# Performance work log

Measured on AMD Instinct MI355X. Metric: run time of the kernel, lower is better.

## Reference

```python
import jax, jax.numpy as jnp
import numpy as np

K = 5          # lbp kernel_size (odd)
POOL = 2       # pool_size
C = 64         # input channels
B, H, W = 8, 256, 256
OUT_CH = 1
NEG_SLOPE = 0.01
LN_EPS = 1e-5


def _idx_pairs(k):
    pairs = [([0, i], [k - 1, k - 1 - i]) for i in range(k)]
    pairs += [([i, k - 1], [k - 1 - i, 0]) for i in range(1, k - 1)]
    return pairs  # 2K-2 pairs


def setup_inputs() -> dict:
    key = jax.random.key(0)
    k1, k2, k3 = jax.random.split(key, 3)
    x = jax.random.normal(k1, (B, C, H, W), dtype=jnp.float32)
    m = 2 * K - 2
    conv_w = jax.random.normal(k2, (OUT_CH, m), dtype=jnp.float32) / np.float32(np.sqrt(m))
    conv_b = jax.random.normal(k3, (OUT_CH,), dtype=jnp.float32) * 0.01
    return {"x": x, "conv_w": conv_w, "conv_b": conv_b}


def _avg_pool(x):
    # torch avg_pool2d(kernel=POOL, stride=1, padding=POOL//2, count_include_pad=True)
    p = POOL // 2
    s = jax.lax.reduce_window(x, jnp.float32(0.0), jax.lax.add,
                              (1, 1, POOL, POOL), (1, 1, 1, 1),
                              ((0, 0), (0, 0), (p, p), (p, p)))
    return s / jnp.float32(POOL * POOL)


def reference(x, conv_w, conv_b):
    xp = _avg_pool(x)                 # [B, C, H+1, W+1]
    # Each lbp kernel plane is (+1 center, -1 at offset) replicated over all C
    # input channels, so the conv reduces to shifts of the channel sum.
    xs = xp.sum(axis=1)               # [B, H', W']
    pad = K // 2
    Hp, Wp = xs.shape[-2], xs.shape[-1]
    xs_pad = jnp.pad(xs, ((0, 0), (pad, pad), (pad, pad)))

    def shift(rc):
        r, c = rc
        return xs_pad[:, r:r + Hp, c:c + Wp]

    # (conv even ch) - (conv odd ch) = shift(idx1) - shift(idx0)
    feats = jnp.stack([shift(b) - shift(a) for a, b in _idx_pairs(K)], axis=1)  # [B, 2K-2, H', W']
    y = jnp.einsum('bmhw,om->bohw', feats, conv_w) + conv_b[None, :, None, None]
    # layer_norm over last two dims, no affine
    mu = y.mean(axis=(-2, -1), keepdims=True)
    var = ((y - mu) ** 2).mean(axis=(-2, -1), keepdims=True)
    y = (y - mu) / jnp.sqrt(var + LN_EPS)
    return jnp.where(y >= 0, y, NEG_SLOPE * y)
```

## Files before the change

### kernel.cpp

```cpp
#include <hip/hip_runtime.h>
#include <math.h>

#define BB 8
#define CC 64
#define HH 256
#define WW 256
#define HP 257
#define NPB (HP * HP)
#define NBLK ((NPB + 255) / 256)

#define SROWS 262
#define SSTR  264
#define SPIMG (SROWS * SSTR)

#define OFF_PART 0
#define OFF_Y    4352
#define OFF_SPAD (OFF_Y + BB * NPB)

#define N_INT (BB * 16384)
#define PAD_PER_IMG 908
#define N_TOT (N_INT + BB * PAD_PER_IMG)

__global__ __launch_bounds__(256) void k_chansum(const float* __restrict__ x,
                                                 float* __restrict__ ws) {
    int tid = blockIdx.x * 256 + threadIdx.x;
    float4* sp4 = reinterpret_cast<float4*>(ws + OFF_SPAD);
    if (tid < N_INT) {
        int b = tid >> 14;
        int p = tid & 16383;
        int i = p >> 6;
        int j4 = p & 63;
        const float4* xp = reinterpret_cast<const float4*>(x)
                           + (size_t)b * (CC * 16384) + p;
        float4 acc = make_float4(0.f, 0.f, 0.f, 0.f);
#pragma unroll 16
        for (int c = 0; c < CC; ++c) {
            float4 v = xp[(size_t)c * 16384];
            acc.x += v.x; acc.y += v.y; acc.z += v.z; acc.w += v.w;
        }
        sp4[b * (SPIMG / 4) + (i + 3) * (SSTR / 4) + 1 + j4] = acc;
    } else {
        int j = tid - N_INT;
        if (j < BB * PAD_PER_IMG) {
            int img = j / PAD_PER_IMG;
            int k = j % PAD_PER_IMG;
            int row, col4;
            if (k < 396) {
                int r = k / 66;
                row = (r < 3) ? r : 256 + r;
                col4 = k % 66;
            } else {
                int k2 = k - 396;
                row = 3 + (k2 >> 1);
                col4 = (k2 & 1) ? 65 : 0;
            }
            sp4[img * (SPIMG / 4) + row * (SSTR / 4) + col4] =
                make_float4(0.f, 0.f, 0.f, 0.f);
        }
    }
}

__device__ __forceinline__ void build_w(const float* __restrict__ cw, float W[6][6]) {
    float T[5][5];
#pragma unroll
    for (int i = 0; i < 5; ++i)
#pragma unroll
        for (int j = 0; j < 5; ++j) T[i][j] = 0.f;
#pragma unroll
    for (int d = 0; d < 5; ++d) { T[0][d] = -cw[d]; T[4][d] = cw[4 - d]; }
    T[1][4] = -cw[5]; T[2][4] = -cw[6]; T[3][4] = -cw[7];
    T[1][0] =  cw[7]; T[2][0] =  cw[6]; T[3][0] =  cw[5];
#pragma unroll
    for (int u = 0; u < 6; ++u)
#pragma unroll
        for (int v = 0; v < 6; ++v) {
            float a = 0.f;
#pragma unroll
            for (int dr = u - 1; dr <= u; ++dr)
#pragma unroll
                for (int dc = v - 1; dc <= v; ++dc)
                    if (dr >= 0 && dr < 5 && dc >= 0 && dc < 5) a += T[dr][dc];
            W[u][v] = 0.25f * a;
        }
}

__global__ __launch_bounds__(256) void k_conv(float* __restrict__ ws,
                                              const float* __restrict__ cw,
                                              const float* __restrict__ cbp) {
    int b = blockIdx.y;
    int e = blockIdx.x * 256 + threadIdx.x;
    float W[6][6];
    build_w(cw, W);
    float y = 0.f;
    if (e < NPB) {
        int h = e / HP, w = e % HP;
        const float* p = ws + OFF_SPAD + b * SPIMG + h * SSTR + w + 1;
        float acc = cbp[0];
#pragma unroll
        for (int u = 0; u < 6; ++u)
#pragma unroll
            for (int v = 0; v < 6; ++v)
                acc += W[u][v] * p[u * SSTR + v];
        y = acc;
        ws[OFF_Y + b * NPB + e] = y;
    }
    float v1 = y, v2 = y * y;
    for (int off = 32; off > 0; off >>= 1) {
        v1 += __shfl_down(v1, off);
        v2 += __shfl_down(v2, off);
    }
    __shared__ float red[8];
    int lane = threadIdx.x & 63, wid = threadIdx.x >> 6;
    if (lane == 0) { red[wid] = v1; red[4 + wid] = v2; }
    __syncthreads();
    if (threadIdx.x == 0) {
        ws[OFF_PART + b * NBLK + blockIdx.x] = red[0] + red[1] + red[2] + red[3];
        ws[OFF_PART + BB * NBLK + b * NBLK + blockIdx.x] =
            red[4] + red[5] + red[6] + red[7];
    }
}

__global__ __launch_bounds__(256) void k_final(const float* __restrict__ ws,
                                               float* __restrict__ out) {
    int b = blockIdx.y;
    float v1 = 0.f, v2 = 0.f;
    for (int i = threadIdx.x; i < NBLK; i += 256) {
        v1 += ws[OFF_PART + b * NBLK + i];
        v2 += ws[OFF_PART + BB * NBLK + b * NBLK + i];
    }
    for (int off = 32; off > 0; off >>= 1) {
        v1 += __shfl_down(v1, off);
        v2 += __shfl_down(v2, off);
    }
    __shared__ float red[8];
    __shared__ float st[2];
    int lane = threadIdx.x & 63, wid = threadIdx.x >> 6;
    if (lane == 0) { red[wid] = v1; red[4 + wid] = v2; }
    __syncthreads();
    if (threadIdx.x == 0) {
        float s1 = red[0] + red[1] + red[2] + red[3];
        float s2 = red[4] + red[5] + red[6] + red[7];
        float mu = s1 / (float)NPB;
        float var = s2 / (float)NPB - mu * mu;
        st[0] = mu;
        st[1] = 1.0f / sqrtf(var + 1e-5f);
    }
    __syncthreads();
    float mu = st[0], rs = st[1];
    int e = blockIdx.x * 256 + threadIdx.x;
    if (e < NPB) {
        float z = (ws[OFF_Y + b * NPB + e] - mu) * rs;
        out[b * NPB + e] = (z >= 0.f) ? z : 0.01f * z;
    }
}

extern "C" void kernel_launch(void* const* d_in, const int* in_sizes, int n_in,
                              void* d_out, int out_size, void* d_ws, size_t ws_size,
                              hipStream_t stream) {
    const float* x  = (const float*)d_in[0];
    const float* cw = (const float*)d_in[1];
    const float* cb = (const float*)d_in[2];
    float* out = (float*)d_out;
    float* ws  = (float*)d_ws;

    k_chansum<<<(N_TOT + 255) / 256, 256, 0, stream>>>(x, ws);
    dim3 g(NBLK, BB);
    k_conv<<<g, 256, 0, stream>>>(ws, cw, cb);
    k_final<<<g, 256, 0, stream>>>(ws, out);
}
```

Measured before the change: 202.3 us.

## Fuse three kernels into one cooperative kernel with grid syncs

Merges the channel-sum, conv and normalize kernels into a single cooperative launch of 512 blocks, separated by grid-wide barriers. Conv results stay in registers across the second barrier, so the intermediate y buffer is never written to or read back from global memory, and two launch gaps disappear. In exchange the channel-sum phase runs on a fixed 512-block grid with a grid-stride loop instead of a grid sized to the work, which may lower memory-level parallelism in that bandwidth-bound phase. Each grid.sync also costs something.

```diff
diff --git a/kernel.cpp b/kernel.cpp
--- a/kernel.cpp
+++ b/kernel.cpp
@@ -1,5 +1,8 @@
 #include <hip/hip_runtime.h>
+#include <hip/hip_cooperative_groups.h>
 #include <math.h>
+
+namespace cg = cooperative_groups;
 
 #define BB 8
 #define CC 64
@@ -7,58 +10,22 @@
 #define WW 256
 #define HP 257
 #define NPB (HP * HP)
-#define NBLK ((NPB + 255) / 256)
 
 #define SROWS 262
 #define SSTR  264
 #define SPIMG (SROWS * SSTR)
 
 #define OFF_PART 0
-#define OFF_Y    4352
-#define OFF_SPAD (OFF_Y + BB * NPB)
+#define OFF_SPAD 4352
+
+#define GRID 512
+#define NTHREADS (GRID * 256)
 
 #define N_INT (BB * 16384)
 #define PAD_PER_IMG 908
 #define N_TOT (N_INT + BB * PAD_PER_IMG)
 
-__global__ __launch_bounds__(256) void k_chansum(const float* __restrict__ x,
-                                                 float* __restrict__ ws) {
-    int tid = blockIdx.x * 256 + threadIdx.x;
-    float4* sp4 = reinterpret_cast<float4*>(ws + OFF_SPAD);
-    if (tid < N_INT) {
-        int b = tid >> 14;
-        int p = tid & 16383;
-        int i = p >> 6;
-        int j4 = p & 63;
-        const float4* xp = reinterpret_cast<const float4*>(x)
-                           + (size_t)b * (CC * 16384) + p;
-        float4 acc = make_float4(0.f, 0.f, 0.f, 0.f);
-#pragma unroll 16
-        for (int c = 0; c < CC; ++c) {
-            float4 v = xp[(size_t)c * 16384];
-            acc.x += v.x; acc.y += v.y; acc.z += v.z; acc.w += v.w;
-        }
-        sp4[b * (SPIMG / 4) + (i + 3) * (SSTR / 4) + 1 + j4] = acc;
-    } else {
-        int j = tid - N_INT;
-        if (j < BB * PAD_PER_IMG) {
-            int img = j / PAD_PER_IMG;
-            int k = j % PAD_PER_IMG;
-            int row, col4;
-            if (k < 396) {
-                int r = k / 66;
-                row = (r < 3) ? r : 256 + r;
-                col4 = k % 66;
-            } else {
-                int k2 = k - 396;
-                row = 3 + (k2 >> 1);
-                col4 = (k2 & 1) ? 65 : 0;
-            }
-            sp4[img * (SPIMG / 4) + row * (SSTR / 4) + col4] =
-                make_float4(0.f, 0.f, 0.f, 0.f);
-        }
-    }
-}
+#define EPB 1033
 
 __device__ __forceinline__ void build_w(const float* __restrict__ cw, float W[6][6]) {
     float T[5][5];
@@ -84,49 +51,82 @@
         }
 }
 
-__global__ __launch_bounds__(256) void k_conv(float* __restrict__ ws,
-                                              const float* __restrict__ cw,
-                                              const float* __restrict__ cbp) {
-    int b = blockIdx.y;
-    int e = blockIdx.x * 256 + threadIdx.x;
+__global__ __launch_bounds__(256) void k_fused(const float* __restrict__ x,
+                                               const float* __restrict__ cw,
+                                               const float* __restrict__ cbp,
+                                               float* __restrict__ ws,
+                                               float* __restrict__ out) {
+    cg::grid_group grid = cg::this_grid();
+    const int tid = threadIdx.x;
+    const int blk = blockIdx.x;
+    const int gtid = blk * 256 + tid;
+
+    float4* sp4 = reinterpret_cast<float4*>(ws + OFF_SPAD);
+    for (int idx = gtid; idx < N_TOT; idx += NTHREADS) {
+        if (idx < N_INT) {
+            int b = idx >> 14;
+            int p = idx & 16383;
+            int i = p >> 6;
+            int j4 = p & 63;
+            const float4* xp = reinterpret_cast<const float4*>(x)
+                               + (size_t)b * (CC * 16384) + p;
+            float4 acc = make_float4(0.f, 0.f, 0.f, 0.f);
+#pragma unroll 16
+            for (int c = 0; c < CC; ++c) {
+                float4 v = xp[(size_t)c * 16384];
+                acc.x += v.x; acc.y += v.y; acc.z += v.z; acc.w += v.w;
+            }
+            sp4[b * (SPIMG / 4) + (i + 3) * (SSTR / 4) + 1 + j4] = acc;
+        } else {
+            int j = idx - N_INT;
+            int img = j / PAD_PER_IMG;
+            int k = j % PAD_PER_IMG;
+            int row, col4;
+            if (k < 396) {
+                int r = k / 66;
+                row = (r < 3) ? r : 256 + r;
+                col4 = k % 66;
+            } else {
+                int k2 = k - 396;
+                row = 3 + (k2 >> 1);
+                col4 = (k2 & 1) ? 65 : 0;
+            }
+            sp4[img * (SPIMG / 4) + row * (SSTR / 4) + col4] =
+                make_float4(0.f, 0.f, 0.f, 0.f);
+        }
+    }
+
+    grid.sync();
+
+    const int bb = blk >> 6;
+    const int sub = blk & 63;
+    const int e_base = sub * EPB;
+    const int e_end = (e_base + EPB < NPB) ? e_base + EPB : NPB;
+
     float W[6][6];
     build_w(cw, W);
-    float y = 0.f;
-    if (e < NPB) {
-        int h = e / HP, w = e % HP;
-        const float* p = ws + OFF_SPAD + b * SPIMG + h * SSTR + w + 1;
-        float acc = cbp[0];
+    const float cb = cbp[0];
+    const float* sbase = ws + OFF_SPAD + bb * SPIMG;
+
+    float yv[5];
+    float v1 = 0.f, v2 = 0.f;
 #pragma unroll
-        for (int u = 0; u < 6; ++u)
+    for (int it = 0; it < 5; ++it) {
+        int e = e_base + it * 256 + tid;
+        float y = 0.f;
+        if (e < e_end) {
+            int h = e / HP, w = e % HP;
+            const float* p = sbase + h * SSTR + w + 1;
+            float acc = cb;
 #pragma unroll
-            for (int v = 0; v < 6; ++v)
-                acc += W[u][v] * p[u * SSTR + v];
-        y = acc;
-        ws[OFF_Y + b * NPB + e] = y;
-    }
-    float v1 = y, v2 = y * y;
-    for (int off = 32; off > 0; off >>= 1) {
-        v1 += __shfl_down(v1, off);
-        v2 += __shfl_down(v2, off);
-    }
-    __shared__ float red[8];
-    int lane = threadIdx.x & 63, wid = threadIdx.x >> 6;
-    if (lane == 0) { red[wid] = v1; red[4 + wid] = v2; }
-    __syncthreads();
-    if (threadIdx.x == 0) {
-        ws[OFF_PART + b * NBLK + blockIdx.x] = red[0] + red[1] + red[2] + red[3];
-        ws[OFF_PART + BB * NBLK + b * NBLK + blockIdx.x] =
-            red[4] + red[5] + red[6] + red[7];
-    }
-}
-
-__global__ __launch_bounds__(256) void k_final(const float* __restrict__ ws,
-                                               float* __restrict__ out) {
-    int b = blockIdx.y;
-    float v1 = 0.f, v2 = 0.f;
-    for (int i = threadIdx.x; i < NBLK; i += 256) {
-        v1 += ws[OFF_PART + b * NBLK + i];
-        v2 += ws[OFF_PART + BB * NBLK + b * NBLK + i];
+            for (int u = 0; u < 6; ++u)
+#pragma unroll
+                for (int v = 0; v < 6; ++v)
+                    acc += W[u][v] * p[u * SSTR + v];
+            y = acc;
+            v1 += y; v2 += y * y;
+        }
+        yv[it] = y;
     }
     for (int off = 32; off > 0; off >>= 1) {
         v1 += __shfl_down(v1, off);
@@ -134,23 +134,43 @@
     }
     __shared__ float red[8];
     __shared__ float st[2];
-    int lane = threadIdx.x & 63, wid = threadIdx.x >> 6;
+    int lane = tid & 63, wid = tid >> 6;
     if (lane == 0) { red[wid] = v1; red[4 + wid] = v2; }
     __syncthreads();
-    if (threadIdx.x == 0) {
-        float s1 = red[0] + red[1] + red[2] + red[3];
-        float s2 = red[4] + red[5] + red[6] + red[7];
-        float mu = s1 / (float)NPB;
-        float var = s2 / (float)NPB - mu * mu;
-        st[0] = mu;
-        st[1] = 1.0f / sqrtf(var + 1e-5f);
+    if (tid == 0) {
+        ws[OFF_PART + blk * 2]     = red[0] + red[1] + red[2] + red[3];
+        ws[OFF_PART + blk * 2 + 1] = red[4] + red[5] + red[6] + red[7];
+    }
+
+    grid.sync();
+
+    float s1 = 0.f, s2 = 0.f;
+    if (tid < 64) {
+        s1 = ws[OFF_PART + (bb * 64 + tid) * 2];
+        s2 = ws[OFF_PART + (bb * 64 + tid) * 2 + 1];
+    }
+    if (wid == 0) {
+        for (int off = 32; off > 0; off >>= 1) {
+            s1 += __shfl_down(s1, off);
+            s2 += __shfl_down(s2, off);
+        }
+        if (tid == 0) {
+            float mu = s1 / (float)NPB;
+            float var = s2 / (float)NPB - mu * mu;
+            st[0] = mu;
+            st[1] = 1.0f / sqrtf(var + 1e-5f);
+        }
     }
     __syncthreads();
-    float mu = st[0], rs = st[1];
-    int e = blockIdx.x * 256 + threadIdx.x;
-    if (e < NPB) {
-        float z = (ws[OFF_Y + b * NPB + e] - mu) * rs;
-        out[b * NPB + e] = (z >= 0.f) ? z : 0.01f * z;
+    const float mu = st[0], rs = st[1];
+    float* ob = out + bb * NPB;
+#pragma unroll
+    for (int it = 0; it < 5; ++it) {
+        int e = e_base + it * 256 + tid;
+        if (e < e_end) {
+            float z = (yv[it] - mu) * rs;
+            ob[e] = (z >= 0.f) ? z : 0.01f * z;
+        }
     }
 }
 
@@ -163,8 +183,7 @@
     float* out = (float*)d_out;
     float* ws  = (float*)d_ws;
 
-    k_chansum<<<(N_TOT + 255) / 256, 256, 0, stream>>>(x, ws);
-    dim3 g(NBLK, BB);
-    k_conv<<<g, 256, 0, stream>>>(ws, cw, cb);
-    k_final<<<g, 256, 0, stream>>>(ws, out);
+    void* args[] = {(void*)&x, (void*)&cw, (void*)&cb, (void*)&ws, (void*)&out};
+    hipLaunchCooperativeKernel((void*)k_fused, dim3(GRID), dim3(256),
+                               args, 0, stream);
 }
```

Result: slower. 318.2 us (+57.3%).

## Split channel sum into two halves, vectorize conv and finalize four pixels per thread

Applied to the files above, without the earlier changes.

The channel-sum kernel now splits the 64 channels into two halves across 1024 blocks with nontemporal loads, which doubles the parallelism over the bandwidth-bound read of x. A new combine kernel adds the two partials and writes the padded image. The conv kernel computes four output pixels per thread from vectorized row loads and writes y into a padded-stride buffer. The finalize kernel processes four pixels per thread and reduces fewer partials. This adds an extra launch and an extra partial-buffer round trip in exchange.

```diff
diff --git a/kernel.cpp b/kernel.cpp
--- a/kernel.cpp
+++ b/kernel.cpp
@@ -1,5 +1,7 @@
 #include <hip/hip_runtime.h>
 #include <math.h>
+
+typedef float vfloat4 __attribute__((ext_vector_type(4)));
 
 #define BB 8
 #define CC 64
@@ -7,56 +9,73 @@
 #define WW 256
 #define HP 257
 #define NPB (HP * HP)
-#define NBLK ((NPB + 255) / 256)
 
 #define SROWS 262
-#define SSTR  264
+#define SSTR  268
 #define SPIMG (SROWS * SSTR)
+#define SSTR4 (SSTR / 4)
+
+#define YSTR 260
+#define YIMG (HP * YSTR)
 
 #define OFF_PART 0
-#define OFF_Y    4352
-#define OFF_SPAD (OFF_Y + BB * NPB)
+#define OFF_Y    2048
+#define OFF_P    536608
+#define OFF_SPAD 1585184
 
 #define N_INT (BB * 16384)
-#define PAD_PER_IMG 908
+#define PAD_PER_IMG 1170
 #define N_TOT (N_INT + BB * PAD_PER_IMG)
+
+#define GPB (HP * 65)
+#define CBLK 66
 
 __global__ __launch_bounds__(256) void k_chansum(const float* __restrict__ x,
                                                  float* __restrict__ ws) {
-    int tid = blockIdx.x * 256 + threadIdx.x;
-    float4* sp4 = reinterpret_cast<float4*>(ws + OFF_SPAD);
-    if (tid < N_INT) {
-        int b = tid >> 14;
-        int p = tid & 16383;
-        int i = p >> 6;
-        int j4 = p & 63;
-        const float4* xp = reinterpret_cast<const float4*>(x)
-                           + (size_t)b * (CC * 16384) + p;
-        float4 acc = make_float4(0.f, 0.f, 0.f, 0.f);
+    int idx = blockIdx.x * 256 + threadIdx.x;
+    int half = idx >> 17;
+    int r = idx & 131071;
+    int b = r >> 14;
+    int p = r & 16383;
+    const vfloat4* xp = reinterpret_cast<const vfloat4*>(x)
+                        + (size_t)b * (CC * 16384) + (size_t)half * (32 * 16384) + p;
+    vfloat4 acc = {0.f, 0.f, 0.f, 0.f};
 #pragma unroll 16
-        for (int c = 0; c < CC; ++c) {
-            float4 v = xp[(size_t)c * 16384];
-            acc.x += v.x; acc.y += v.y; acc.z += v.z; acc.w += v.w;
+    for (int c = 0; c < 32; ++c) {
+        vfloat4 v = __builtin_nontemporal_load(&xp[(size_t)c * 16384]);
+        acc += v;
+    }
+    reinterpret_cast<vfloat4*>(ws + OFF_P)[half * 131072 + r] = acc;
+}
+
+__global__ __launch_bounds__(256) void k_combine(float* __restrict__ ws) {
+    int idx = blockIdx.x * 256 + threadIdx.x;
+    if (idx >= N_TOT) return;
+    vfloat4* sp4 = reinterpret_cast<vfloat4*>(ws + OFF_SPAD);
+    if (idx < N_INT) {
+        const vfloat4* p04 = reinterpret_cast<const vfloat4*>(ws + OFF_P);
+        vfloat4 s = p04[idx] + p04[131072 + idx];
+        int b = idx >> 14;
+        int p = idx & 16383;
+        int i = p >> 6, j4 = p & 63;
+        sp4[b * (SPIMG / 4) + (i + 3) * SSTR4 + 1 + j4] = s;
+    } else {
+        int k = idx - N_INT;
+        int img = k / PAD_PER_IMG;
+        int k2 = k % PAD_PER_IMG;
+        int row, col4;
+        if (k2 < 402) {
+            int rr = k2 / 67;
+            row = (rr < 3) ? rr : 256 + rr;
+            col4 = k2 % 67;
+        } else {
+            int k3 = k2 - 402;
+            row = 3 + k3 / 3;
+            int m = k3 % 3;
+            col4 = (m == 0) ? 0 : 64 + m;
         }
-        sp4[b * (SPIMG / 4) + (i + 3) * (SSTR / 4) + 1 + j4] = acc;
-    } else {
-        int j = tid - N_INT;
-        if (j < BB * PAD_PER_IMG) {
-            int img = j / PAD_PER_IMG;
-            int k = j % PAD_PER_IMG;
-            int row, col4;
-            if (k < 396) {
-                int r = k / 66;
-                row = (r < 3) ? r : 256 + r;
-                col4 = k % 66;
-            } else {
-                int k2 = k - 396;
-                row = 3 + (k2 >> 1);
-                col4 = (k2 & 1) ? 65 : 0;
-            }
-            sp4[img * (SPIMG / 4) + row * (SSTR / 4) + col4] =
-                make_float4(0.f, 0.f, 0.f, 0.f);
-        }
+        vfloat4 z = {0.f, 0.f, 0.f, 0.f};
+        sp4[img * (SPIMG / 4) + row * SSTR4 + col4] = z;
     }
 }
 
@@ -88,23 +107,34 @@
                                               const float* __restrict__ cw,
                                               const float* __restrict__ cbp) {
     int b = blockIdx.y;
-    int e = blockIdx.x * 256 + threadIdx.x;
-    float W[6][6];
-    build_w(cw, W);
-    float y = 0.f;
-    if (e < NPB) {
-        int h = e / HP, w = e % HP;
-        const float* p = ws + OFF_SPAD + b * SPIMG + h * SSTR + w + 1;
-        float acc = cbp[0];
-#pragma unroll
-        for (int u = 0; u < 6; ++u)
-#pragma unroll
-            for (int v = 0; v < 6; ++v)
-                acc += W[u][v] * p[u * SSTR + v];
-        y = acc;
-        ws[OFF_Y + b * NPB + e] = y;
-    }
-    float v1 = y, v2 = y * y;
+    int g = blockIdx.x * 256 + threadIdx.x;
+    float v1 = 0.f, v2 = 0.f;
+    if (g < GPB) {
+        float W[6][6];
+        build_w(cw, W);
+        const float cb = cbp[0];
+        int h = g / 65, wg = g % 65, w0 = wg * 4;
+        const float* sb = ws + OFF_SPAD + b * SPIMG + h * SSTR + w0;
+        float acc[4] = {cb, cb, cb, cb};
+#pragma unroll
+        for (int u = 0; u < 6; ++u) {
+            const vfloat4* rp = reinterpret_cast<const vfloat4*>(sb + u * SSTR);
+            vfloat4 A = rp[0], Bv = rp[1], Cv = rp[2];
+            float r[12] = {A.x, A.y, A.z, A.w, Bv.x, Bv.y, Bv.z, Bv.w,
+                           Cv.x, Cv.y, Cv.z, Cv.w};
+#pragma unroll
+            for (int j = 0; j < 4; ++j)
+#pragma unroll
+                for (int v = 0; v < 6; ++v)
+                    acc[j] += W[u][v] * r[1 + j + v];
+        }
+        vfloat4 yo = {acc[0], acc[1], acc[2], acc[3]};
+        reinterpret_cast<vfloat4*>(ws + OFF_Y + b * YIMG + h * YSTR + w0)[0] = yo;
+        int nv = (wg == 64) ? 1 : 4;
+#pragma unroll
+        for (int j = 0; j < 4; ++j)
+            if (j < nv) { v1 += acc[j]; v2 += acc[j] * acc[j]; }
+    }
     for (int off = 32; off > 0; off >>= 1) {
         v1 += __shfl_down(v1, off);
         v2 += __shfl_down(v2, off);
@@ -114,19 +144,20 @@
     if (lane == 0) { red[wid] = v1; red[4 + wid] = v2; }
     __syncthreads();
     if (threadIdx.x == 0) {
-        ws[OFF_PART + b * NBLK + blockIdx.x] = red[0] + red[1] + red[2] + red[3];
-        ws[OFF_PART + BB * NBLK + b * NBLK + blockIdx.x] =
-            red[4] + red[5] + red[6] + red[7];
+        int pb = b * CBLK + blockIdx.x;
+        ws[OFF_PART + 2 * pb]     = red[0] + red[1] + red[2] + red[3];
+        ws[OFF_PART + 2 * pb + 1] = red[4] + red[5] + red[6] + red[7];
     }
 }
 
 __global__ __launch_bounds__(256) void k_final(const float* __restrict__ ws,
                                                float* __restrict__ out) {
     int b = blockIdx.y;
+    int tid = threadIdx.x;
     float v1 = 0.f, v2 = 0.f;
-    for (int i = threadIdx.x; i < NBLK; i += 256) {
-        v1 += ws[OFF_PART + b * NBLK + i];
-        v2 += ws[OFF_PART + BB * NBLK + b * NBLK + i];
+    if (tid < CBLK) {
+        v1 = ws[OFF_PART + 2 * (b * CBLK + tid)];
+        v2 = ws[OFF_PART + 2 * (b * CBLK + tid) + 1];
     }
     for (int off = 32; off > 0; off >>= 1) {
         v1 += __shfl_down(v1, off);
@@ -134,10 +165,10 @@
     }
     __shared__ float red[8];
     __shared__ float st[2];
-    int lane = threadIdx.x & 63, wid = threadIdx.x >> 6;
+    int lane = tid & 63, wid = tid >> 6;
     if (lane == 0) { red[wid] = v1; red[4 + wid] = v2; }
     __syncthreads();
-    if (threadIdx.x == 0) {
+    if (tid == 0) {
         float s1 = red[0] + red[1] + red[2] + red[3];
         float s2 = red[4] + red[5] + red[6] + red[7];
         float mu = s1 / (float)NPB;
@@ -146,11 +177,21 @@
         st[1] = 1.0f / sqrtf(var + 1e-5f);
     }
     __syncthreads();
-    float mu = st[0], rs = st[1];
-    int e = blockIdx.x * 256 + threadIdx.x;
-    if (e < NPB) {
-        float z = (ws[OFF_Y + b * NPB + e] - mu) * rs;
-        out[b * NPB + e] = (z >= 0.f) ? z : 0.01f * z;
+    const float mu = st[0], rs = st[1];
+    int g = blockIdx.x * 256 + tid;
+    if (g < GPB) {
+        int h = g / 65, wg = g % 65, w0 = wg * 4;
+        vfloat4 yv = reinterpret_cast<const vfloat4*>(ws + OFF_Y + b * YIMG
+                                                      + h * YSTR + w0)[0];
+        float yr[4] = {yv.x, yv.y, yv.z, yv.w};
+        int nv = (wg == 64) ? 1 : 4;
+        float* ob = out + b * NPB + h * HP + w0;
+#pragma unroll
+        for (int j = 0; j < 4; ++j)
+            if (j < nv) {
+                float z = (yr[j] - mu) * rs;
+                ob[j] = (z >= 0.f) ? z : 0.01f * z;
+            }
     }
 }
 
@@ -163,8 +204,9 @@
     float* out = (float*)d_out;
     float* ws  = (float*)d_ws;
 
-    k_chansum<<<(N_TOT + 255) / 256, 256, 0, stream>>>(x, ws);
-    dim3 g(NBLK, BB);
+    k_chansum<<<1024, 256, 0, stream>>>(x, ws);
+    k_combine<<<(N_TOT + 255) / 256, 256, 0, stream>>>(ws);
+    dim3 g(CBLK, BB);
     k_conv<<<g, 256, 0, stream>>>(ws, cw, cb);
     k_final<<<g, 256, 0, stream>>>(ws, out);
 }
```

Measured after the change: 195.4 us. 1.04x faster.
